# Performance work log

Measured on AMD Instinct MI355X. Metric: run time of the kernel, lower is better.

The kernel has to match this reference:

```python
import jax, jax.numpy as jnp
import numpy as np

N_NODES = 50000
N_EDGES = 640000
F_IN = 64
EDGE_DIM = 16
HID = 128
N_LAYERS = 3
N_CLASSES = 2
NUM_GRAPHS = 64
BN_EPS = 1e-5


def setup_inputs() -> dict:
    key = jax.random.key(0)
    ks = jax.random.split(key, 20)
    s = 0.05
    inp = {
        "x": jax.random.normal(ks[0], (N_NODES, F_IN), dtype=jnp.float32),
        "edge_index": jax.random.randint(ks[1], (2, N_EDGES), 0, N_NODES, dtype=jnp.int32),
        "edge_attr": jax.random.normal(ks[2], (N_EDGES, EDGE_DIM), dtype=jnp.float32),
        "batch": jnp.sort(jax.random.randint(ks[3], (N_NODES,), 0, NUM_GRAPHS, dtype=jnp.int32)),
        # node encoder
        "enc_W": jax.random.normal(ks[4], (F_IN, HID), dtype=jnp.float32) * s,
        "enc_b": jnp.zeros((HID,), dtype=jnp.float32),
        # per-layer GINEConv params (stacked over layers)
        "edge_W": jax.random.normal(ks[5], (N_LAYERS, EDGE_DIM, HID), dtype=jnp.float32) * s,
        "edge_b": jnp.zeros((N_LAYERS, HID), dtype=jnp.float32),
        "mlp_W1": jax.random.normal(ks[6], (N_LAYERS, HID, HID), dtype=jnp.float32) * s,
        "mlp_b1": jnp.zeros((N_LAYERS, HID), dtype=jnp.float32),
        "mlp_W2": jax.random.normal(ks[7], (N_LAYERS, HID, HID), dtype=jnp.float32) * s,
        "mlp_b2": jnp.zeros((N_LAYERS, HID), dtype=jnp.float32),
        "bn_gamma": jnp.ones((N_LAYERS, HID), dtype=jnp.float32),
        "bn_beta": jnp.zeros((N_LAYERS, HID), dtype=jnp.float32),
        # classification head
        "head_W1": jax.random.normal(ks[8], (HID, HID), dtype=jnp.float32) * s,
        "head_b1": jnp.zeros((HID,), dtype=jnp.float32),
        "head_W2": jax.random.normal(ks[9], (HID, N_CLASSES), dtype=jnp.float32) * s,
        "head_b2": jnp.zeros((N_CLASSES,), dtype=jnp.float32),
    }
    return inp


def reference(x, edge_index, edge_attr, batch, enc_W, enc_b, edge_W, edge_b,
              mlp_W1, mlp_b1, mlp_W2, mlp_b2, bn_gamma, bn_beta,
              head_W1, head_b1, head_W2, head_b2):
    src, dst = edge_index[0], edge_index[1]  # message flows src -> dst
    h = x @ enc_W + enc_b  # [N, HID]
    for l in range(N_LAYERS):
        # GINEConv: msg = ReLU(x_src + Lin(edge_attr)); aggr = scatter_add at dst
        e = edge_attr @ edge_W[l] + edge_b[l]          # [E, HID]
        msg = jax.nn.relu(h[src] + e)                  # [E, HID]
        agg = jax.ops.segment_sum(msg, dst, num_segments=N_NODES)
        z = h + agg  # (1 + eps) * x + aggr, eps = 0
        # node MLP: Linear-ReLU-Linear
        z = jax.nn.relu(z @ mlp_W1[l] + mlp_b1[l]) @ mlp_W2[l] + mlp_b2[l]
        # BatchNorm1d (training-mode batch stats) + ReLU (dropout = identity)
        mean = jnp.mean(z, axis=0)
        var = jnp.var(z, axis=0)
        z = bn_gamma[l] * (z - mean) * jax.lax.rsqrt(var + BN_EPS) + bn_beta[l]
        h = jax.nn.relu(z)
    # global_add_pool over graphs
    g = jax.ops.segment_sum(h, batch, num_segments=NUM_GRAPHS)  # [G, HID]
    out = jax.nn.relu(g @ head_W1 + head_b1) @ head_W2 + head_b2
    return out  # [G, N_CLASSES]
```

## Files before the change

kernel.cpp:

```cpp
#include <hip/hip_runtime.h>
#include <hip/hip_bf16.h>

#define N_NODES 50000
#define N_EDGES 640000
#define F_IN 64
#define EDGE_DIM 16
#define HID 128
#define N_LAYERS 3
#define NUM_GRAPHS 64
#define BN_EPS 1e-5f

typedef __attribute__((ext_vector_type(8))) short short8;
typedef __attribute__((ext_vector_type(4))) float f32x4;
typedef __attribute__((ext_vector_type(2))) __fp16 half2v;
typedef __attribute__((ext_vector_type(8))) __fp16 half8;

__device__ __forceinline__ float bfl(unsigned int u) {
    unsigned int v = u << 16; float f; __builtin_memcpy(&f, &v, 4); return f;
}
__device__ __forceinline__ float bfh(unsigned int u) {
    unsigned int v = u & 0xffff0000u; float f; __builtin_memcpy(&f, &v, 4); return f;
}
__device__ __forceinline__ unsigned int f2bf(float f) {
    unsigned int v; __builtin_memcpy(&v, &f, 4);
    v += 0x7fffu + ((v >> 16) & 1u);
    return v >> 16;
}
__device__ __forceinline__ unsigned int pack2(float lo, float hi) {
    return f2bf(lo) | (f2bf(hi) << 16);
}
__device__ __forceinline__ unsigned int pkh(float a, float b) {
    half2v h = __builtin_amdgcn_cvt_pkrtz(a, b);
    unsigned int u; __builtin_memcpy(&u, &h, 4); return u;
}

__global__ void k_hist(const int* __restrict__ dst, int* __restrict__ deg) {
    int e = blockIdx.x * 256 + threadIdx.x;
    atomicAdd(&deg[dst[e]], 1);
}

__global__ void k_blockred(const int* __restrict__ deg, int* __restrict__ bsums) {
    __shared__ int s[256];
    int i = blockIdx.x * 256 + threadIdx.x;
    int v = (i < N_NODES) ? deg[i] : 0;
    s[threadIdx.x] = v;
    __syncthreads();
    for (int off = 128; off > 0; off >>= 1) {
        if (threadIdx.x < off) s[threadIdx.x] += s[threadIdx.x + off];
        __syncthreads();
    }
    if (threadIdx.x == 0) bsums[blockIdx.x] = s[0];
}

__global__ void k_scan_bsums(int* __restrict__ bsums, int nb) {
    __shared__ int s[256];
    const int tid = threadIdx.x;
    const int v = (tid < nb) ? bsums[tid] : 0;
    s[tid] = v;
    __syncthreads();
    for (int off = 1; off < 256; off <<= 1) {
        int t = 0;
        if (tid >= off) t = s[tid - off];
        __syncthreads();
        s[tid] += t;
        __syncthreads();
    }
    if (tid < nb) bsums[tid] = s[tid] - v;
}

__global__ void k_scan_blocks(int* __restrict__ deg_rowptr, const int* __restrict__ bsums,
                              int* __restrict__ cursor) {
    __shared__ int s[256];
    int tid = threadIdx.x;
    int i = blockIdx.x * 256 + tid;
    int v = (i < N_NODES) ? deg_rowptr[i] : 0;
    s[tid] = v;
    __syncthreads();
    for (int off = 1; off < 256; off <<= 1) {
        int t = 0;
        if (tid >= off) t = s[tid - off];
        __syncthreads();
        s[tid] += t;
        __syncthreads();
    }
    int excl = s[tid] - v + bsums[blockIdx.x];
    if (i < N_NODES) {
        deg_rowptr[i] = excl;
        cursor[i] = excl;
    }
    if (i == N_NODES - 1) deg_rowptr[N_NODES] = N_EDGES;
}

__global__ void k_fill(const int* __restrict__ dst, int* __restrict__ cursor,
                       int* __restrict__ elist) {
    int e = blockIdx.x * 256 + threadIdx.x;
    int p = atomicAdd(&cursor[dst[e]], 1);
    elist[p] = e;
}

__global__ __launch_bounds__(256) void k_gather(const int* __restrict__ elist,
                                                const int* __restrict__ esrc,
                                                const float* __restrict__ eattr,
                                                int* __restrict__ src_s,
                                                uint4* __restrict__ eattr_h) {
    const int base = blockIdx.x * 1024;
    const int tid = threadIdx.x;
    int p[4], eid[4];
#pragma unroll
    for (int j = 0; j < 4; ++j) p[j] = base + tid + j * 256;
#pragma unroll
    for (int j = 0; j < 4; ++j) eid[j] = elist[p[j]];
    int sv[4];
#pragma unroll
    for (int j = 0; j < 4; ++j) sv[j] = esrc[eid[j]];
    float4 a[4][4];
#pragma unroll
    for (int j = 0; j < 4; ++j) {
        const float* ep = eattr + (size_t)eid[j] * EDGE_DIM;
        a[j][0] = *(const float4*)ep;
        a[j][1] = *(const float4*)(ep + 4);
        a[j][2] = *(const float4*)(ep + 8);
        a[j][3] = *(const float4*)(ep + 12);
    }
#pragma unroll
    for (int j = 0; j < 4; ++j) {
        src_s[p[j]] = sv[j];
        eattr_h[p[j] * 2] = make_uint4(pkh(a[j][0].x, a[j][0].y), pkh(a[j][0].z, a[j][0].w),
                                       pkh(a[j][1].x, a[j][1].y), pkh(a[j][1].z, a[j][1].w));
        eattr_h[p[j] * 2 + 1] = make_uint4(pkh(a[j][2].x, a[j][2].y), pkh(a[j][2].z, a[j][2].w),
                                           pkh(a[j][3].x, a[j][3].y), pkh(a[j][3].z, a[j][3].w));
    }
}

__global__ void k_pack(const float* __restrict__ W1, const float* __restrict__ W2,
                       const float* __restrict__ encW, const float* __restrict__ eW,
                       const float* __restrict__ eb2,
                       unsigned short* __restrict__ wp, unsigned short* __restrict__ wpe,
                       unsigned short* __restrict__ wekf) {
    const int t = blockIdx.x * 256 + threadIdx.x;
    if (t < 12288) {
        const int mat = t >> 11;
        const int r = t & 2047;
        const int kstep = r >> 9;
        const int ntile = (r >> 6) & 7;
        const int lane = r & 63;
        const float* W = (mat < 3) ? (W1 + mat * 16384) : (W2 + (mat - 3) * 16384);
        const int kbase = kstep * 32 + ((lane >> 4) << 3);
        const int n = ntile * 16 + (lane & 15);
        unsigned int o[4];
#pragma unroll
        for (int jj = 0; jj < 4; ++jj)
            o[jj] = pack2(W[(kbase + 2 * jj) * HID + n], W[(kbase + 2 * jj + 1) * HID + n]);
        *(uint4*)(wp + (size_t)mat * 16384 + (((kstep << 3) + ntile) * 64 + lane) * 8) =
            make_uint4(o[0], o[1], o[2], o[3]);
    } else if (t < 13312) {
        const int r = t - 12288;
        const int kstep = r >> 9;
        const int ntile = (r >> 6) & 7;
        const int lane = r & 63;
        const int kbase = kstep * 32 + ((lane >> 4) << 3);
        const int n = ntile * 16 + (lane & 15);
        unsigned int o[4];
#pragma unroll
        for (int jj = 0; jj < 4; ++jj)
            o[jj] = pack2(encW[(kbase + 2 * jj) * HID + n], encW[(kbase + 2 * jj + 1) * HID + n]);
        *(uint4*)(wpe + (((kstep << 3) + ntile) * 64 + lane) * 8) =
            make_uint4(o[0], o[1], o[2], o[3]);
    } else {
        const int r = t - 13312;
        const int l = r >> 10;
        const int rr = r & 1023;
        const int nt = rr >> 7;
        const int lane = (rr >> 1) & 63;
        const int hf = rr & 1;
        const int qq = lane >> 4;
        const int f = ((lane & 15) << 3) + nt;
        float v[4];
#pragma unroll
        for (int j = 0; j < 4; ++j) {
            const int k = (qq << 3) + (hf << 2) + j;
            v[j] = (k < 16) ? eW[(l * EDGE_DIM + k) * HID + f]
                            : ((k == 16) ? eb2[l * HID + f] : 0.f);
        }
        *(uint2*)(wekf + (((l * 8 + nt) * 64 + lane) * 8) + (hf << 2)) =
            make_uint2(pkh(v[0], v[1]), pkh(v[2], v[3]));
    }
}

__global__ __launch_bounds__(256, 3) void k_encm(const float* __restrict__ x,
                                                 const unsigned short* __restrict__ wpe,
                                                 const float* __restrict__ b,
                                                 unsigned short* __restrict__ hb) {
    const int tid = threadIdx.x;
    const int w = tid >> 6, lane = tid & 63;
    const int q = lane >> 4, l15 = lane & 15;
    const int row0 = blockIdx.x * 64 + w * 16;
    const int ar = min(row0 + l15, N_NODES - 1);
    const float* xp = x + (size_t)ar * F_IN + q * 8;
    f32x4 acc[8];
#pragma unroll
    for (int nt = 0; nt < 8; ++nt) acc[nt] = (f32x4){0.f, 0.f, 0.f, 0.f};
#pragma unroll
    for (int ks = 0; ks < 2; ++ks) {
        const float4 v0 = *(const float4*)(xp + ks * 32);
        const float4 v1 = *(const float4*)(xp + ks * 32 + 4);
        unsigned int u[4] = {pack2(v0.x, v0.y), pack2(v0.z, v0.w),
                             pack2(v1.x, v1.y), pack2(v1.z, v1.w)};
        short8 a; __builtin_memcpy(&a, u, 16);
#pragma unroll
        for (int nt = 0; nt < 8; ++nt) {
            const short8 bf = *(const short8*)(wpe + (((ks << 3) + nt) * 64 + lane) * 8);
            acc[nt] = __builtin_amdgcn_mfma_f32_16x16x32_bf16(a, bf, acc[nt], 0, 0, 0);
        }
    }
    const int rowb = row0 + q * 4;
#pragma unroll
    for (int nt = 0; nt < 8; ++nt) {
        const float bias = b[nt * 16 + l15];
        const int cc = nt * 16 + l15;
#pragma unroll
        for (int reg = 0; reg < 4; ++reg) {
            const int r = rowb + reg;
            if (r < N_NODES)
                hb[(size_t)r * HID + cc] = (unsigned short)f2bf(acc[nt][reg] + bias);
        }
    }
}

__global__ __launch_bounds__(256, 2) void k_agg(const unsigned short* __restrict__ hrow,
                                                const int* __restrict__ src_s,
                                                const uint4* __restrict__ eattr_h,
                                                const unsigned short* __restrict__ wekf,
                                                const int* __restrict__ row_ptr,
                                                const float* __restrict__ bnst,
                                                const float* __restrict__ gamma,
                                                const float* __restrict__ beta,
                                                const int bnmode,
                                                unsigned int* __restrict__ zb32) {
    const int lane = threadIdx.x & 63;
    const int wv = threadIdx.x >> 6;
    const int q = lane >> 4, l15 = lane & 15;
    const int f0 = l15 * 8;

    half8 Bf[8];
#pragma unroll
    for (int nt = 0; nt < 8; ++nt) {
        uint4 u = *(const uint4*)(wekf + (nt * 64 + lane) * 8);
        __builtin_memcpy(&Bf[nt], &u, 16);
    }

    float sc[8], sh[8];
    float rlo = -3.4e38f;
    if (bnmode) {
        rlo = 0.f;
        const float invN = 1.0f / (float)N_NODES;
#pragma unroll
        for (int j = 0; j < 8; ++j) {
            const int f = f0 + j;
            const float m = bnst[f] * invN;
            const float v = fmaxf(bnst[128 + f] * invN - m * m, 0.f);
            const float r = rsqrtf(v + BN_EPS);
            sc[j] = gamma[f] * r;
            sh[j] = fmaf(-m, sc[j], beta[f]);
        }
    } else {
#pragma unroll
        for (int j = 0; j < 8; ++j) { sc[j] = 1.f; sh[j] = 0.f; }
    }

    const int wid = blockIdx.x * 4 + wv;
    const int n0 = wid * 5;

    for (int i = 0; i < 5; ++i) {
        const int n = n0 + i;
        const int base = __builtin_amdgcn_readfirstlane(row_ptr[n]);
        const int deg  = __builtin_amdgcn_readfirstlane(row_ptr[n + 1]) - base;

        float accf[8];
#pragma unroll
        for (int j = 0; j < 8; ++j) accf[j] = 0.f;

        const int ntile = (deg + 15) >> 4;
        for (int t = 0; t < ntile; ++t) {
            const int e0 = t * 16;
            uint4 au = make_uint4(0u, 0u, 0u, 0u);
            if (q < 2) {
                const int ea = min(e0 + l15, deg - 1);
                au = eattr_h[(size_t)(base + ea) * 2 + q];
            } else if (q == 2) {
                au.x = 0x3C00u;
            }
            half8 Af; __builtin_memcpy(&Af, &au, 16);

            int sv[4];
#pragma unroll
            for (int r = 0; r < 4; ++r)
                sv[r] = src_s[base + min(e0 + q * 4 + r, deg - 1)];
            uint4 hg[4];
#pragma unroll
            for (int r = 0; r < 4; ++r)
                hg[r] = *(const uint4*)(hrow + (size_t)sv[r] * HID + f0);

            f32x4 acc[8];
#pragma unroll
            for (int nt = 0; nt < 8; ++nt) {
                acc[nt] = (f32x4){0.f, 0.f, 0.f, 0.f};
                acc[nt] = __builtin_amdgcn_mfma_f32_16x16x32_f16(Af, Bf[nt], acc[nt], 0, 0, 0);
            }

#pragma unroll
            for (int r = 0; r < 4; ++r) {
                const float m = (e0 + q * 4 + r < deg) ? 1.f : 0.f;
                const unsigned int* hu = (const unsigned int*)&hg[r];
#pragma unroll
                for (int p = 0; p < 4; ++p) {
                    const float hA = fmaxf(fmaf(bfl(hu[p]), sc[2 * p],     sh[2 * p]),     rlo);
                    const float hB = fmaxf(fmaf(bfh(hu[p]), sc[2 * p + 1], sh[2 * p + 1]), rlo);
                    accf[2 * p]     = fmaf(m, fmaxf(hA + acc[2 * p][r],     0.f), accf[2 * p]);
                    accf[2 * p + 1] = fmaf(m, fmaxf(hB + acc[2 * p + 1][r], 0.f), accf[2 * p + 1]);
                }
            }
        }

#pragma unroll
        for (int j = 0; j < 8; ++j) {
            accf[j] += __shfl_xor(accf[j], 16, 64);
            accf[j] += __shfl_xor(accf[j], 32, 64);
        }

        if (q == 0) {
            const uint4 hs = *(const uint4*)(hrow + (size_t)n * HID + f0);
            const unsigned int* hu = (const unsigned int*)&hs;
            unsigned int o[4];
#pragma unroll
            for (int p = 0; p < 4; ++p) {
                const float hA = fmaxf(fmaf(bfl(hu[p]), sc[2 * p],     sh[2 * p]),     rlo);
                const float hB = fmaxf(fmaf(bfh(hu[p]), sc[2 * p + 1], sh[2 * p + 1]), rlo);
                o[p] = pack2(hA + accf[2 * p], hB + accf[2 * p + 1]);
            }
            *(uint4*)(zb32 + (size_t)n * 64 + l15 * 4) = make_uint4(o[0], o[1], o[2], o[3]);
        }
    }
}

#define Z1LD 136

__global__ __launch_bounds__(256, 3) void k_mlp(const unsigned short* __restrict__ zb,
                                                const unsigned short* __restrict__ w1p,
                                                const float* __restrict__ b1,
                                                const unsigned short* __restrict__ w2p,
                                                const float* __restrict__ b2,
                                                unsigned short* __restrict__ z2b,
                                                float* __restrict__ bn) {
    __shared__ unsigned short z1s[64 * Z1LD];
    __shared__ float redA[512];
    __shared__ float redB[512];
    const int tid = threadIdx.x;
    const int w = tid >> 6, lane = tid & 63;
    const int q = lane >> 4, l15 = lane & 15;
    const int row0 = blockIdx.x * 64 + w * 16;

    const int ar = min(row0 + l15, N_NODES - 1);
    const unsigned short* aptr = zb + (size_t)ar * HID + q * 8;

    f32x4 acc[8];
#pragma unroll
    for (int nt = 0; nt < 8; ++nt) acc[nt] = (f32x4){0.f, 0.f, 0.f, 0.f};

#pragma unroll
    for (int ks = 0; ks < 4; ++ks) {
        const short8 a = *(const short8*)(aptr + ks * 32);
#pragma unroll
        for (int nt = 0; nt < 8; ++nt) {
            const short8 b = *(const short8*)(w1p + (((ks << 3) + nt) * 64 + lane) * 8);
            acc[nt] = __builtin_amdgcn_mfma_f32_16x16x32_bf16(a, b, acc[nt], 0, 0, 0);
        }
    }
    {
        const int lr0 = w * 16 + q * 4;
#pragma unroll
        for (int nt = 0; nt < 8; ++nt) {
            const float bias = b1[nt * 16 + l15];
            const int cc = nt * 16 + l15;
#pragma unroll
            for (int reg = 0; reg < 4; ++reg) {
                const float v = fmaxf(acc[nt][reg] + bias, 0.f);
                z1s[(lr0 + reg) * Z1LD + cc] = (unsigned short)f2bf(v);
            }
        }
    }
#pragma unroll
    for (int nt = 0; nt < 8; ++nt) acc[nt] = (f32x4){0.f, 0.f, 0.f, 0.f};
    const unsigned short* a2p = &z1s[(w * 16 + l15) * Z1LD + q * 8];
#pragma unroll
    for (int ks = 0; ks < 4; ++ks) {
        const short8 a = *(const short8*)(a2p + ks * 32);
#pragma unroll
        for (int nt = 0; nt < 8; ++nt) {
            const short8 b = *(const short8*)(w2p + (((ks << 3) + nt) * 64 + lane) * 8);
            acc[nt] = __builtin_amdgcn_mfma_f32_16x16x32_bf16(a, b, acc[nt], 0, 0, 0);
        }
    }
    float s[8], sq[8];
    const int rowb = row0 + q * 4;
#pragma unroll
    for (int nt = 0; nt < 8; ++nt) {
        const float bias = b2[nt * 16 + l15];
        const int cc = nt * 16 + l15;
        float ls = 0.f, lq = 0.f;
#pragma unroll
        for (int reg = 0; reg < 4; ++reg) {
            const int r = rowb + reg;
            const float v = acc[nt][reg] + bias;
            if (r < N_NODES) {
                z2b[(size_t)r * HID + cc] = (unsigned short)f2bf(v);
                ls += v;
                lq = fmaf(v, v, lq);
            }
        }
        s[nt] = ls; sq[nt] = lq;
    }
#pragma unroll
    for (int nt = 0; nt < 8; ++nt) {
        s[nt] += __shfl_xor(s[nt], 16, 64);
        s[nt] += __shfl_xor(s[nt], 32, 64);
        sq[nt] += __shfl_xor(sq[nt], 16, 64);
        sq[nt] += __shfl_xor(sq[nt], 32, 64);
    }
    if (lane < 16) {
#pragma unroll
        for (int nt = 0; nt < 8; ++nt) {
            redA[w * 128 + nt * 16 + lane] = s[nt];
            redB[w * 128 + nt * 16 + lane] = sq[nt];
        }
    }
    __syncthreads();
    if (tid < 128) {
        float t = redA[tid] + redA[128 + tid] + redA[256 + tid] + redA[384 + tid];
        atomicAdd(&bn[tid], t);
    } else {
        const int c = tid - 128;
        float t = redB[c] + redB[128 + c] + redB[256 + c] + redB[384 + c];
        atomicAdd(&bn[128 + c], t);
    }
}

__global__ void k_pool(const unsigned short* __restrict__ z2b, const int* __restrict__ batch,
                       const float* __restrict__ bnst, const float* __restrict__ gamma,
                       const float* __restrict__ beta, float* __restrict__ g) {
    const int f = threadIdx.x;
    const float invN = 1.0f / (float)N_NODES;
    const float m = bnst[f] * invN;
    const float var = fmaxf(bnst[128 + f] * invN - m * m, 0.f);
    const float r = rsqrtf(var + BN_EPS);
    const float sc = gamma[f] * r;
    const float sh = fmaf(-m, sc, beta[f]);

    const int n0 = blockIdx.x * 128;
    const int nend = min(n0 + 128, N_NODES);
    float acc = 0.f;
    int cur = batch[n0];
    for (int n = n0; n < nend; ++n) {
        const int bb = batch[n];
        if (bb != cur) {
            atomicAdd(&g[cur * HID + f], acc);
            acc = 0.f;
            cur = bb;
        }
        const float raw = bfl((unsigned int)z2b[n * HID + f]);
        acc += fmaxf(fmaf(raw, sc, sh), 0.f);
    }
    atomicAdd(&g[cur * HID + f], acc);
}

__global__ void k_head1(const float* __restrict__ g, const float* __restrict__ W,
                        const float* __restrict__ b, float* __restrict__ g1) {
    const int idx = blockIdx.x * 256 + threadIdx.x;
    const int r = idx >> 7, c = idx & 127;
    float acc = b[c];
    for (int k = 0; k < 128; ++k) acc = fmaf(g[r * HID + k], W[k * HID + c], acc);
    g1[idx] = fmaxf(acc, 0.f);
}

__global__ void k_head2(const float* __restrict__ g1, const float* __restrict__ W,
                        const float* __restrict__ b, float* __restrict__ out) {
    const int idx = threadIdx.x;
    const int r = idx >> 1, c = idx & 1;
    float acc = b[c];
    for (int k = 0; k < 128; ++k) acc = fmaf(g1[r * HID + k], W[k * 2 + c], acc);
    out[idx] = acc;
}

extern "C" void kernel_launch(void* const* d_in, const int* in_sizes, int n_in,
                              void* d_out, int out_size, void* d_ws, size_t ws_size,
                              hipStream_t stream) {
    const float* x     = (const float*)d_in[0];
    const int*   ei    = (const int*)d_in[1];
    const float* eattr = (const float*)d_in[2];
    const int*   batch = (const int*)d_in[3];
    const float* encW  = (const float*)d_in[4];
    const float* encb  = (const float*)d_in[5];
    const float* eW    = (const float*)d_in[6];
    const float* eb    = (const float*)d_in[7];
    const float* W1    = (const float*)d_in[8];
    const float* b1    = (const float*)d_in[9];
    const float* W2    = (const float*)d_in[10];
    const float* b2    = (const float*)d_in[11];
    const float* gam   = (const float*)d_in[12];
    const float* bet   = (const float*)d_in[13];
    const float* hW1   = (const float*)d_in[14];
    const float* hb1   = (const float*)d_in[15];
    const float* hW2   = (const float*)d_in[16];
    const float* hb2   = (const float*)d_in[17];
    float* out = (float*)d_out;

    float* ws = (float*)d_ws;
    unsigned short* z2b = (unsigned short*)ws;
    float* bn  = ws + 3200000;
    float* g   = ws + 3200256;
    float* g1  = ws + 3208448;
    unsigned short* hb = (unsigned short*)(ws + 3216640);
    unsigned int* zb32 = (unsigned int*)(ws + 6416640);
    unsigned short* wekf = (unsigned short*)(ws + 9616640);
    int* row_ptr = (int*)(ws + 11216640);
    int* cursor  = row_ptr + N_NODES + 1;
    int* elist   = cursor + N_NODES;
    int* bsums   = elist + N_EDGES;
    int* src_s   = bsums + 256;
    uint4* eattr_h = (uint4*)(ws + 12596900);
    unsigned short* wp  = (unsigned short*)(ws + 17716900);
    unsigned short* wpe = (unsigned short*)(ws + 17766100);

    const int* esrc = ei;
    const int* edst = ei + N_EDGES;

    hipMemsetAsync(row_ptr, 0, (N_NODES + 1) * sizeof(int), stream);
    k_hist<<<N_EDGES / 256, 256, 0, stream>>>(edst, row_ptr);
    k_blockred<<<196, 256, 0, stream>>>(row_ptr, bsums);
    k_scan_bsums<<<1, 256, 0, stream>>>(bsums, 196);
    k_scan_blocks<<<196, 256, 0, stream>>>(row_ptr, bsums, cursor);
    k_fill<<<N_EDGES / 256, 256, 0, stream>>>(edst, cursor, elist);
    k_gather<<<N_EDGES / 1024, 256, 0, stream>>>(elist, esrc, eattr, src_s, eattr_h);

    k_pack<<<64, 256, 0, stream>>>(W1, W2, encW, eW, eb, wp, wpe, wekf);

    k_encm<<<782, 256, 0, stream>>>(x, wpe, encb, hb);

    for (int l = 0; l < N_LAYERS; ++l) {
        const unsigned short* hrow = (l == 0) ? hb : z2b;
        k_agg<<<2500, 256, 0, stream>>>(hrow, src_s, eattr_h,
                                        wekf + (size_t)l * 4096, row_ptr,
                                        bn, gam + (l ? (l - 1) * HID : 0),
                                        bet + (l ? (l - 1) * HID : 0),
                                        (l > 0) ? 1 : 0, zb32);
        hipMemsetAsync(bn, 0, 256 * sizeof(float), stream);
        k_mlp<<<782, 256, 0, stream>>>((const unsigned short*)zb32,
                                       wp + (size_t)l * 16384, b1 + l * HID,
                                       wp + (size_t)(3 + l) * 16384, b2 + l * HID,
                                       z2b, bn);
    }

    hipMemsetAsync(g, 0, NUM_GRAPHS * HID * sizeof(float), stream);
    k_pool<<<391, 128, 0, stream>>>(z2b, batch, bn, gam + 2 * HID, bet + 2 * HID, g);
    k_head1<<<32, 256, 0, stream>>>(g, hW1, hb1, g1);
    k_head2<<<1, 128, 0, stream>>>(g1, hW2, hb2, out);
}
```

Measured before the change: 538.4 us.

## Split BatchNorm apply into separate kernel and assign one node per wave in aggregation

```diff
diff --git a/kernel.cpp b/kernel.cpp
--- a/kernel.cpp
+++ b/kernel.cpp
@@ -227,15 +227,40 @@
     }
 }
 
+__global__ __launch_bounds__(256) void k_bn(const unsigned short* __restrict__ z,
+                                            const float* __restrict__ bnst,
+                                            const float* __restrict__ gamma,
+                                            const float* __restrict__ beta,
+                                            unsigned short* __restrict__ hb2) {
+    const int idx = blockIdx.x * 256 + threadIdx.x;
+    const int f0 = (idx * 8) & 127;
+    const float invN = 1.0f / (float)N_NODES;
+    uint4 v = *(const uint4*)(z + (size_t)idx * 8);
+    const unsigned int* u = (const unsigned int*)&v;
+    unsigned int o[4];
+#pragma unroll
+    for (int p = 0; p < 4; ++p) {
+        const int f = f0 + 2 * p;
+        const float m0 = bnst[f] * invN;
+        const float m1 = bnst[f + 1] * invN;
+        const float v0 = fmaxf(bnst[128 + f] * invN - m0 * m0, 0.f);
+        const float v1 = fmaxf(bnst[128 + f + 1] * invN - m1 * m1, 0.f);
+        const float r0 = rsqrtf(v0 + BN_EPS), r1 = rsqrtf(v1 + BN_EPS);
+        const float sc0 = gamma[f] * r0, sc1 = gamma[f + 1] * r1;
+        const float sh0 = fmaf(-m0, sc0, beta[f]);
+        const float sh1 = fmaf(-m1, sc1, beta[f + 1]);
+        const float a = fmaxf(fmaf(bfl(u[p]), sc0, sh0), 0.f);
+        const float b = fmaxf(fmaf(bfh(u[p]), sc1, sh1), 0.f);
+        o[p] = pack2(a, b);
+    }
+    *(uint4*)(hb2 + (size_t)idx * 8) = make_uint4(o[0], o[1], o[2], o[3]);
+}
+
 __global__ __launch_bounds__(256, 2) void k_agg(const unsigned short* __restrict__ hrow,
                                                 const int* __restrict__ src_s,
                                                 const uint4* __restrict__ eattr_h,
                                                 const unsigned short* __restrict__ wekf,
                                                 const int* __restrict__ row_ptr,
-                                                const float* __restrict__ bnst,
-                                                const float* __restrict__ gamma,
-                                                const float* __restrict__ beta,
-                                                const int bnmode,
                                                 unsigned int* __restrict__ zb32) {
     const int lane = threadIdx.x & 63;
     const int wv = threadIdx.x >> 6;
@@ -249,37 +274,15 @@
         __builtin_memcpy(&Bf[nt], &u, 16);
     }
 
-    float sc[8], sh[8];
-    float rlo = -3.4e38f;
-    if (bnmode) {
-        rlo = 0.f;
-        const float invN = 1.0f / (float)N_NODES;
-#pragma unroll
-        for (int j = 0; j < 8; ++j) {
-            const int f = f0 + j;
-            const float m = bnst[f] * invN;
-            const float v = fmaxf(bnst[128 + f] * invN - m * m, 0.f);
-            const float r = rsqrtf(v + BN_EPS);
-            sc[j] = gamma[f] * r;
-            sh[j] = fmaf(-m, sc[j], beta[f]);
-        }
-    } else {
-#pragma unroll
-        for (int j = 0; j < 8; ++j) { sc[j] = 1.f; sh[j] = 0.f; }
-    }
-
-    const int wid = blockIdx.x * 4 + wv;
-    const int n0 = wid * 5;
-
-    for (int i = 0; i < 5; ++i) {
-        const int n = n0 + i;
-        const int base = __builtin_amdgcn_readfirstlane(row_ptr[n]);
-        const int deg  = __builtin_amdgcn_readfirstlane(row_ptr[n + 1]) - base;
-
-        float accf[8];
-#pragma unroll
-        for (int j = 0; j < 8; ++j) accf[j] = 0.f;
-
+    const int n = blockIdx.x * 4 + wv;
+    const int base = __builtin_amdgcn_readfirstlane(row_ptr[n]);
+    const int deg  = __builtin_amdgcn_readfirstlane(row_ptr[n + 1]) - base;
+
+    float accf[8];
+#pragma unroll
+    for (int j = 0; j < 8; ++j) accf[j] = 0.f;
+
+    if (deg > 0) {
         const int ntile = (deg + 15) >> 4;
         for (int t = 0; t < ntile; ++t) {
             const int e0 = t * 16;
@@ -314,32 +317,27 @@
                 const unsigned int* hu = (const unsigned int*)&hg[r];
 #pragma unroll
                 for (int p = 0; p < 4; ++p) {
-                    const float hA = fmaxf(fmaf(bfl(hu[p]), sc[2 * p],     sh[2 * p]),     rlo);
-                    const float hB = fmaxf(fmaf(bfh(hu[p]), sc[2 * p + 1], sh[2 * p + 1]), rlo);
-                    accf[2 * p]     = fmaf(m, fmaxf(hA + acc[2 * p][r],     0.f), accf[2 * p]);
-                    accf[2 * p + 1] = fmaf(m, fmaxf(hB + acc[2 * p + 1][r], 0.f), accf[2 * p + 1]);
+                    accf[2 * p]     = fmaf(m, fmaxf(bfl(hu[p]) + acc[2 * p][r],     0.f), accf[2 * p]);
+                    accf[2 * p + 1] = fmaf(m, fmaxf(bfh(hu[p]) + acc[2 * p + 1][r], 0.f), accf[2 * p + 1]);
                 }
             }
         }
-
-#pragma unroll
-        for (int j = 0; j < 8; ++j) {
-            accf[j] += __shfl_xor(accf[j], 16, 64);
-            accf[j] += __shfl_xor(accf[j], 32, 64);
-        }
-
-        if (q == 0) {
-            const uint4 hs = *(const uint4*)(hrow + (size_t)n * HID + f0);
-            const unsigned int* hu = (const unsigned int*)&hs;
-            unsigned int o[4];
-#pragma unroll
-            for (int p = 0; p < 4; ++p) {
-                const float hA = fmaxf(fmaf(bfl(hu[p]), sc[2 * p],     sh[2 * p]),     rlo);
-                const float hB = fmaxf(fmaf(bfh(hu[p]), sc[2 * p + 1], sh[2 * p + 1]), rlo);
-                o[p] = pack2(hA + accf[2 * p], hB + accf[2 * p + 1]);
-            }
-            *(uint4*)(zb32 + (size_t)n * 64 + l15 * 4) = make_uint4(o[0], o[1], o[2], o[3]);
-        }
+    }
+
+#pragma unroll
+    for (int j = 0; j < 8; ++j) {
+        accf[j] += __shfl_xor(accf[j], 16, 64);
+        accf[j] += __shfl_xor(accf[j], 32, 64);
+    }
+
+    if (q == 0) {
+        const uint4 hs = *(const uint4*)(hrow + (size_t)n * HID + f0);
+        const unsigned int* hu = (const unsigned int*)&hs;
+        unsigned int o[4];
+#pragma unroll
+        for (int p = 0; p < 4; ++p)
+            o[p] = pack2(bfl(hu[p]) + accf[2 * p], bfh(hu[p]) + accf[2 * p + 1]);
+        *(uint4*)(zb32 + (size_t)n * 64 + l15 * 4) = make_uint4(o[0], o[1], o[2], o[3]);
     }
 }
 
@@ -511,7 +509,7 @@
     const float* hW1   = (const float*)d_in[14];
     const float* hb1   = (const float*)d_in[15];
     const float* hW2   = (const float*)d_in[16];
-    const float* hb2   = (const float*)d_in[17];
+    const float* hb2w  = (const float*)d_in[17];
     float* out = (float*)d_out;
 
     float* ws = (float*)d_ws;
@@ -519,17 +517,18 @@
     float* bn  = ws + 3200000;
     float* g   = ws + 3200256;
     float* g1  = ws + 3208448;
-    unsigned short* hb = (unsigned short*)(ws + 3216640);
-    unsigned int* zb32 = (unsigned int*)(ws + 6416640);
-    unsigned short* wekf = (unsigned short*)(ws + 9616640);
-    int* row_ptr = (int*)(ws + 11216640);
+    unsigned short* hb  = (unsigned short*)(ws + 3216640);
+    unsigned int* zb32  = (unsigned int*)(ws + 6416640);
+    unsigned short* hb2 = (unsigned short*)(ws + 9616640);
+    unsigned short* wekf = (unsigned short*)(ws + 12816640);
+    unsigned short* wp  = (unsigned short*)(ws + 12822784);
+    unsigned short* wpe = (unsigned short*)(ws + 12871936);
+    int* row_ptr = (int*)(ws + 12876032);
     int* cursor  = row_ptr + N_NODES + 1;
     int* elist   = cursor + N_NODES;
     int* bsums   = elist + N_EDGES;
     int* src_s   = bsums + 256;
-    uint4* eattr_h = (uint4*)(ws + 12596900);
-    unsigned short* wp  = (unsigned short*)(ws + 17716900);
-    unsigned short* wpe = (unsigned short*)(ws + 17766100);
+    uint4* eattr_h = (uint4*)(ws + 14256292);
 
     const int* esrc = ei;
     const int* edst = ei + N_EDGES;
@@ -547,12 +546,16 @@
     k_encm<<<782, 256, 0, stream>>>(x, wpe, encb, hb);
 
     for (int l = 0; l < N_LAYERS; ++l) {
-        const unsigned short* hrow = (l == 0) ? hb : z2b;
-        k_agg<<<2500, 256, 0, stream>>>(hrow, src_s, eattr_h,
-                                        wekf + (size_t)l * 4096, row_ptr,
-                                        bn, gam + (l ? (l - 1) * HID : 0),
-                                        bet + (l ? (l - 1) * HID : 0),
-                                        (l > 0) ? 1 : 0, zb32);
+        const unsigned short* hrow;
+        if (l == 0) {
+            hrow = hb;
+        } else {
+            k_bn<<<3125, 256, 0, stream>>>(z2b, bn, gam + (l - 1) * HID,
+                                           bet + (l - 1) * HID, hb2);
+            hrow = hb2;
+        }
+        k_agg<<<12500, 256, 0, stream>>>(hrow, src_s, eattr_h,
+                                         wekf + (size_t)l * 4096, row_ptr, zb32);
         hipMemsetAsync(bn, 0, 256 * sizeof(float), stream);
         k_mlp<<<782, 256, 0, stream>>>((const unsigned short*)zb32,
                                        wp + (size_t)l * 16384, b1 + l * HID,
@@ -563,5 +566,5 @@
     hipMemsetAsync(g, 0, NUM_GRAPHS * HID * sizeof(float), stream);
     k_pool<<<391, 128, 0, stream>>>(z2b, batch, bn, gam + 2 * HID, bet + 2 * HID, g);
     k_head1<<<32, 256, 0, stream>>>(g, hW1, hb1, g1);
-    k_head2<<<1, 128, 0, stream>>>(g1, hW2, hb2, out);
-}
+    k_head2<<<1, 128, 0, stream>>>(g1, hW2, hb2w, out);
+}
```

Result: no change. 533.2 us (-1.0%).
